# Kernel tuning notes

Hardware: AMD Instinct MI355X
Metric: run time of the kernel (lower is better)

## Reference

```python
import jax, jax.numpy as jnp
import numpy as np

EMB_DIM = 2048
USER_DIM = 256
NUM_EXPERTS = 64
TOP_K = 8
N_TOKENS = 16384


def setup_inputs() -> dict:
    key = jax.random.key(0)
    k_h, k_u, k_w = jax.random.split(key, 3)
    h = jax.random.normal(k_h, (N_TOKENS, EMB_DIM), dtype=jnp.float32)
    u = jax.random.normal(k_u, (N_TOKENS, USER_DIM), dtype=jnp.float32)
    # nn.Linear weight is [out, in]; we store transposed [in, out] for x @ W
    W = jax.random.normal(k_w, (EMB_DIM + USER_DIM, NUM_EXPERTS), dtype=jnp.float32) * (1.0 / np.sqrt(EMB_DIM + USER_DIM))
    b = jnp.zeros((NUM_EXPERTS,), dtype=jnp.float32)
    return {"h": h, "u": u, "W": W, "b": b}


def reference(h, u, W, b):
    # gate logits: [N, E]
    g = jnp.concatenate([h, u], axis=-1) @ W + b
    w = jax.nn.softmax(g, axis=-1)
    # top-k mask + renormalize (top_k < num_experts)
    _, top_idx = jax.lax.top_k(w, TOP_K)                       # [N, k]
    mask = jax.nn.one_hot(top_idx, NUM_EXPERTS, dtype=w.dtype).sum(axis=-2)  # [N, E]
    w = w * mask
    w = w / (w.sum(axis=-1, keepdims=True) + 1e-9)
    return w
```

## Files before the change

### kernel.cpp

```cpp
#include <hip/hip_runtime.h>

#define EMB 2048
#define UDIM 256
#define KTOT 2304
#define NE 64
#define TOPK 8
#define TPB 64
#define KQ 4
#define EWN 4
#define ESL 16
#define KCH (KTOT / KQ)
#define LP 65

__global__ __launch_bounds__(1024, 4)
void gate_fused(const float* __restrict__ h, const float* __restrict__ u,
                const float* __restrict__ W, const float* __restrict__ b,
                float* __restrict__ out) {
  __shared__ float slab[TPB * LP];

  const int lane = threadIdx.x & 63;
  const int wid  = __builtin_amdgcn_readfirstlane(threadIdx.x >> 6);
  const int kq = wid >> 2;
  const int ew = wid & 3;
  const int tok0 = blockIdx.x * TPB;
  const int token = tok0 + lane;

  float acc[ESL];
#pragma unroll
  for (int j = 0; j < ESL; ++j) acc[j] = 0.f;

  const float* __restrict__ xrow_h = h + (size_t)token * EMB;
  const float* __restrict__ xrow_u = u + (size_t)token * UDIM;

  auto run = [&](const float* __restrict__ xp, const float* __restrict__ wp,
                 int len) {
    float2 xc = *(const float2*)xp;
    float4 wc[2][4];
#pragma unroll
    for (int kk = 0; kk < 2; ++kk)
#pragma unroll
      for (int j = 0; j < 4; ++j)
        wc[kk][j] = *(const float4*)(wp + kk * NE + 4 * j);

    const int iters = len / 2 - 1;
    for (int i = 0; i < iters; ++i) {
      const float* xn_p = xp + 2 * (i + 1);
      const float* wn_p = wp + (size_t)2 * (i + 1) * NE;
      float2 xn = *(const float2*)xn_p;
      float4 wn[2][4];
#pragma unroll
      for (int kk = 0; kk < 2; ++kk)
#pragma unroll
        for (int j = 0; j < 4; ++j)
          wn[kk][j] = *(const float4*)(wn_p + kk * NE + 4 * j);
#pragma unroll
      for (int kk = 0; kk < 2; ++kk) {
        const float xv = kk ? xc.y : xc.x;
#pragma unroll
        for (int j = 0; j < 4; ++j) {
          acc[4 * j + 0] = __builtin_fmaf(xv, wc[kk][j].x, acc[4 * j + 0]);
          acc[4 * j + 1] = __builtin_fmaf(xv, wc[kk][j].y, acc[4 * j + 1]);
          acc[4 * j + 2] = __builtin_fmaf(xv, wc[kk][j].z, acc[4 * j + 2]);
          acc[4 * j + 3] = __builtin_fmaf(xv, wc[kk][j].w, acc[4 * j + 3]);
        }
      }
      xc = xn;
#pragma unroll
      for (int kk = 0; kk < 2; ++kk)
#pragma unroll
        for (int j = 0; j < 4; ++j) wc[kk][j] = wn[kk][j];
    }
#pragma unroll
    for (int kk = 0; kk < 2; ++kk) {
      const float xv = kk ? xc.y : xc.x;
#pragma unroll
      for (int j = 0; j < 4; ++j) {
        acc[4 * j + 0] = __builtin_fmaf(xv, wc[kk][j].x, acc[4 * j + 0]);
        acc[4 * j + 1] = __builtin_fmaf(xv, wc[kk][j].y, acc[4 * j + 1]);
        acc[4 * j + 2] = __builtin_fmaf(xv, wc[kk][j].z, acc[4 * j + 2]);
        acc[4 * j + 3] = __builtin_fmaf(xv, wc[kk][j].w, acc[4 * j + 3]);
      }
    }
  };

  const int k0 = kq * KCH;
  const float* wbase = W + (size_t)k0 * NE + ew * ESL;
  if (kq < 3) {
    run(xrow_h + k0, wbase, KCH);
  } else {
    run(xrow_h + 1728, wbase, EMB - 1728);
    run(xrow_u, W + (size_t)EMB * NE + ew * ESL, UDIM);
  }

  for (int ph = 0; ph < KQ; ++ph) {
    if (kq == ph) {
      float* srow = slab + lane * LP + ew * ESL;
      if (ph == 0) {
#pragma unroll
        for (int j = 0; j < ESL; ++j) srow[j] = acc[j];
      } else {
#pragma unroll
        for (int j = 0; j < ESL; ++j) srow[j] += acc[j];
      }
    }
    __syncthreads();
  }

  const float bias = b[lane];
#pragma unroll
  for (int tt = 0; tt < 4; ++tt) {
    const int t = wid * 4 + tt;
    float g = slab[t * LP + lane] + bias;

    float m = g;
#pragma unroll
    for (int off = 32; off > 0; off >>= 1)
      m = fmaxf(m, __shfl_xor(m, off));
    float p = __expf(g - m);
    float s = p;
#pragma unroll
    for (int off = 32; off > 0; off >>= 1)
      s += __shfl_xor(s, off);
    const float pn = p / s;

    float v = pn;
    float topsum = 0.f;
    int sel = 0;
    for (int r = 0; r < TOPK; ++r) {
      float mv = v;
      int mi = lane;
#pragma unroll
      for (int off = 32; off > 0; off >>= 1) {
        const float ov = __shfl_xor(mv, off);
        const int oi = __shfl_xor(mi, off);
        if (ov > mv || (ov == mv && oi < mi)) { mv = ov; mi = oi; }
      }
      topsum += mv;
      if (lane == mi) { sel = 1; v = -1.f; }
    }

    out[(size_t)(tok0 + t) * NE + lane] =
        sel ? pn / (topsum + 1e-9f) : 0.f;
  }
}

extern "C" void kernel_launch(void* const* d_in, const int* in_sizes, int n_in,
                              void* d_out, int out_size, void* d_ws, size_t ws_size,
                              hipStream_t stream) {
  const float* h = (const float*)d_in[0];
  const float* u = (const float*)d_in[1];
  const float* W = (const float*)d_in[2];
  const float* b = (const float*)d_in[3];
  float* out = (float*)d_out;

  const int n_tokens = in_sizes[0] / EMB;
  const int n_blocks = n_tokens / TPB;

  hipLaunchKernelGGL(gate_fused, dim3(n_blocks), dim3(1024), 0, stream,
                     h, u, W, b, out);
}
```

Measured before the change: 285.6 us.

## Stage token tiles in double-buffered LDS with coalesced loads, split K per window

Before, each lane streamed its own token row straight from global memory, a per-lane strided access. Now the block cooperatively loads 64x64 windows of h and u into a padded LDS tile with coalesced float4 loads, double-buffered so the next window's load overlaps the current window's FMAs. The K split across waves now happens inside each window rather than as four contiguous K quarters. This costs one block-wide barrier per window (36 in total) and extra LDS traffic, and the same LDS buffer is reused for the final cross-wave reduction.

```diff
diff --git a/kernel.cpp b/kernel.cpp
--- a/kernel.cpp
+++ b/kernel.cpp
@@ -6,35 +6,53 @@
 #define NE 64
 #define TOPK 8
 #define TPB 64
-#define KQ 4
-#define EWN 4
+#define LP 65
+#define BK 64
+#define NWIN (KTOT / BK)
 #define ESL 16
-#define KCH (KTOT / KQ)
-#define LP 65
 
 __global__ __launch_bounds__(1024, 4)
 void gate_fused(const float* __restrict__ h, const float* __restrict__ u,
                 const float* __restrict__ W, const float* __restrict__ b,
                 float* __restrict__ out) {
-  __shared__ float slab[TPB * LP];
+  __shared__ float xt[2][TPB * LP];
 
-  const int lane = threadIdx.x & 63;
-  const int wid  = __builtin_amdgcn_readfirstlane(threadIdx.x >> 6);
-  const int kq = wid >> 2;
-  const int ew = wid & 3;
+  const int tid = threadIdx.x;
+  const int lane = tid & 63;
+  const int wid = __builtin_amdgcn_readfirstlane(tid >> 6);
+  const int kq = wid & 3;
+  const int ew = wid >> 2;
   const int tok0 = blockIdx.x * TPB;
-  const int token = tok0 + lane;
+
+  const int stok = tid >> 4;
+  const int sseg = (tid & 15) * 4;
 
   float acc[ESL];
 #pragma unroll
   for (int j = 0; j < ESL; ++j) acc[j] = 0.f;
 
-  const float* __restrict__ xrow_h = h + (size_t)token * EMB;
-  const float* __restrict__ xrow_u = u + (size_t)token * UDIM;
+  {
+    float4 v = *(const float4*)(h + (size_t)(tok0 + stok) * EMB + sseg);
+    float* dst = &xt[0][stok * LP + sseg];
+    dst[0] = v.x; dst[1] = v.y; dst[2] = v.z; dst[3] = v.w;
+  }
+  __syncthreads();
 
-  auto run = [&](const float* __restrict__ xp, const float* __restrict__ wp,
-                 int len) {
-    float2 xc = *(const float2*)xp;
+  const int xbase = lane * LP + kq * 16;
+  int p = 0;
+  for (int w = 0; w < NWIN; ++w) {
+    float4 v;
+    if (w + 1 < NWIN) {
+      const int kn = (w + 1) * BK;
+      const float* src = (kn < EMB)
+          ? h + (size_t)(tok0 + stok) * EMB + kn + sseg
+          : u + (size_t)(tok0 + stok) * UDIM + (kn - EMB) + sseg;
+      v = *(const float4*)src;
+    }
+
+    const float* wp = W + (size_t)(w * BK + kq * 16) * NE + ew * ESL;
+    const float* xp = &xt[p][xbase];
+
     float4 wc[2][4];
 #pragma unroll
     for (int kk = 0; kk < 2; ++kk)
@@ -42,57 +60,51 @@
       for (int j = 0; j < 4; ++j)
         wc[kk][j] = *(const float4*)(wp + kk * NE + 4 * j);
 
-    const int iters = len / 2 - 1;
-    for (int i = 0; i < iters; ++i) {
-      const float* xn_p = xp + 2 * (i + 1);
-      const float* wn_p = wp + (size_t)2 * (i + 1) * NE;
-      float2 xn = *(const float2*)xn_p;
+#pragma unroll
+    for (int pr = 0; pr < 8; ++pr) {
       float4 wn[2][4];
+      if (pr < 7) {
+        const float* wq = wp + (size_t)(2 * pr + 2) * NE;
 #pragma unroll
-      for (int kk = 0; kk < 2; ++kk)
+        for (int kk = 0; kk < 2; ++kk)
 #pragma unroll
-        for (int j = 0; j < 4; ++j)
-          wn[kk][j] = *(const float4*)(wn_p + kk * NE + 4 * j);
-#pragma unroll
-      for (int kk = 0; kk < 2; ++kk) {
-        const float xv = kk ? xc.y : xc.x;
-#pragma unroll
-        for (int j = 0; j < 4; ++j) {
-          acc[4 * j + 0] = __builtin_fmaf(xv, wc[kk][j].x, acc[4 * j + 0]);
-          acc[4 * j + 1] = __builtin_fmaf(xv, wc[kk][j].y, acc[4 * j + 1]);
-          acc[4 * j + 2] = __builtin_fmaf(xv, wc[kk][j].z, acc[4 * j + 2]);
-          acc[4 * j + 3] = __builtin_fmaf(xv, wc[kk][j].w, acc[4 * j + 3]);
-        }
+          for (int j = 0; j < 4; ++j)
+            wn[kk][j] = *(const float4*)(wq + kk * NE + 4 * j);
       }
-      xc = xn;
-#pragma unroll
-      for (int kk = 0; kk < 2; ++kk)
-#pragma unroll
-        for (int j = 0; j < 4; ++j) wc[kk][j] = wn[kk][j];
-    }
-#pragma unroll
-    for (int kk = 0; kk < 2; ++kk) {
-      const float xv = kk ? xc.y : xc.x;
+      const float x0 = xp[2 * pr];
+      const float x1 = xp[2 * pr + 1];
 #pragma unroll
       for (int j = 0; j < 4; ++j) {
-        acc[4 * j + 0] = __builtin_fmaf(xv, wc[kk][j].x, acc[4 * j + 0]);
-        acc[4 * j + 1] = __builtin_fmaf(xv, wc[kk][j].y, acc[4 * j + 1]);
-        acc[4 * j + 2] = __builtin_fmaf(xv, wc[kk][j].z, acc[4 * j + 2]);
-        acc[4 * j + 3] = __builtin_fmaf(xv, wc[kk][j].w, acc[4 * j + 3]);
+        acc[4 * j + 0] = __builtin_fmaf(x0, wc[0][j].x, acc[4 * j + 0]);
+        acc[4 * j + 1] = __builtin_fmaf(x0, wc[0][j].y, acc[4 * j + 1]);
+        acc[4 * j + 2] = __builtin_fmaf(x0, wc[0][j].z, acc[4 * j + 2]);
+        acc[4 * j + 3] = __builtin_fmaf(x0, wc[0][j].w, acc[4 * j + 3]);
+      }
+#pragma unroll
+      for (int j = 0; j < 4; ++j) {
+        acc[4 * j + 0] = __builtin_fmaf(x1, wc[1][j].x, acc[4 * j + 0]);
+        acc[4 * j + 1] = __builtin_fmaf(x1, wc[1][j].y, acc[4 * j + 1]);
+        acc[4 * j + 2] = __builtin_fmaf(x1, wc[1][j].z, acc[4 * j + 2]);
+        acc[4 * j + 3] = __builtin_fmaf(x1, wc[1][j].w, acc[4 * j + 3]);
+      }
+      if (pr < 7) {
+#pragma unroll
+        for (int kk = 0; kk < 2; ++kk)
+#pragma unroll
+          for (int j = 0; j < 4; ++j) wc[kk][j] = wn[kk][j];
       }
     }
-  };
 
-  const int k0 = kq * KCH;
-  const float* wbase = W + (size_t)k0 * NE + ew * ESL;
-  if (kq < 3) {
-    run(xrow_h + k0, wbase, KCH);
-  } else {
-    run(xrow_h + 1728, wbase, EMB - 1728);
-    run(xrow_u, W + (size_t)EMB * NE + ew * ESL, UDIM);
+    if (w + 1 < NWIN) {
+      float* dst = &xt[1 - p][stok * LP + sseg];
+      dst[0] = v.x; dst[1] = v.y; dst[2] = v.z; dst[3] = v.w;
+    }
+    __syncthreads();
+    p ^= 1;
   }
 
-  for (int ph = 0; ph < KQ; ++ph) {
+  float* slab = xt[0];
+  for (int ph = 0; ph < 4; ++ph) {
     if (kq == ph) {
       float* srow = slab + lane * LP + ew * ESL;
       if (ph == 0) {
@@ -116,18 +128,18 @@
 #pragma unroll
     for (int off = 32; off > 0; off >>= 1)
       m = fmaxf(m, __shfl_xor(m, off));
-    float p = __expf(g - m);
-    float s = p;
+    float pexp = __expf(g - m);
+    float s = pexp;
 #pragma unroll
     for (int off = 32; off > 0; off >>= 1)
       s += __shfl_xor(s, off);
-    const float pn = p / s;
+    const float pn = pexp / s;
 
-    float v = pn;
+    float vv = pn;
     float topsum = 0.f;
     int sel = 0;
     for (int r = 0; r < TOPK; ++r) {
-      float mv = v;
+      float mv = vv;
       int mi = lane;
 #pragma unroll
       for (int off = 32; off > 0; off >>= 1) {
@@ -136,7 +148,7 @@
         if (ov > mv || (ov == mv && oi < mi)) { mv = ov; mi = oi; }
       }
       topsum += mv;
-      if (lane == mi) { sel = 1; v = -1.f; }
+      if (lane == mi) { sel = 1; vv = -1.f; }
     }
 
     out[(size_t)(tok0 + t) * NE + lane] =
```

After: 293.8 us. 1.03x slower.
